# Optimization experiments

Measured on AMD Instinct MI355X. Metric: run time of the kernel, lower is better.

Reference implementation:

```python
import jax, jax.numpy as jnp
import numpy as np

NBINS = (128, 64, 32)
N_REGIONS = 5000
N_REGIONS_OI = 500
N_POINTS = 262144
SUM_H = sum(NBINS)            # 224
SUM_W = sum(n - 1 for n in NBINS)  # 221


def _spline_level(x, uw_region, uh_pt, local_ix):
    """One quadratic-spline level.
    x: [N] inputs in [0,1); uw_region: [R, n-1] region unnormalized widths;
    uh_pt: [N, n] per-point unnormalized heights (embedding + delta);
    local_ix: [N] int mapping points -> rows of uw_region.
    """
    # region-level widths / bin locations (calculate_widths / calculate_bin_locations)
    widths = jax.nn.softmax(uw_region, axis=-1)                # [R, n-1]
    bl = jnp.cumsum(widths, axis=-1)
    bl = bl.at[:, -1].set(1.0)
    bin_locations = jnp.pad(bl, ((0, 0), (1, 0)))              # [R, n]

    # gather per point (index_select(0, local_region_ix))
    widths_pt = widths[local_ix]                               # [N, n-1]
    bin_loc_pt = bin_locations[local_ix]                       # [N, n]

    # calculate_heights: exp then normalize so trapezoid integral == 1
    he = jnp.exp(uh_pt)                                        # [N, n]
    area = jnp.sum(0.5 * (he[:, :-1] + he[:, 1:]) * widths_pt, axis=-1, keepdims=True)
    heights = he / area                                        # [N, n]

    # calculate_bin_left_cdf
    cdf = jnp.cumsum(0.5 * (heights[:, :-1] + heights[:, 1:]) * widths_pt, axis=-1)
    cdf = cdf.at[:, -1].set(1.0)
    bin_left_cdf = jnp.pad(cdf, ((0, 0), (1, 0)))              # [N, n]

    # searchsorted(bin_locations, x, side='left') - 1, clamped to valid bins
    n = bin_loc_pt.shape[-1]
    bin_idx = jnp.clip(jnp.sum(bin_loc_pt < x[:, None], axis=-1) - 1, 0, n - 2)  # [N]

    take = lambda a, i: jnp.take_along_axis(a, i[:, None], axis=-1)[:, 0]
    in_loc = take(bin_loc_pt, bin_idx)
    in_w = take(widths_pt, bin_idx)
    in_cdf = take(bin_left_cdf, bin_idx)
    h_l = take(heights, bin_idx)
    h_r = take(heights, bin_idx + 1)

    alpha = (x - in_loc) / in_w
    a = 0.5 * (h_r - h_l) * in_w
    b = h_l * in_w
    out = a * alpha * alpha + b * alpha + in_cdf
    logabsdet = jnp.log(alpha * (h_r - h_l) + h_l)
    return out, logabsdet


def setup_inputs() -> dict:
    key = jax.random.key(0)
    k1, k2, k3, k4, k5, k6 = jax.random.split(key, 6)
    x = jax.random.uniform(k1, (N_POINTS,), dtype=jnp.float32)
    regions_oi = jax.random.randint(k2, (N_REGIONS_OI,), 0, N_REGIONS, dtype=jnp.int32)
    local_region_ix = jax.random.randint(k3, (N_POINTS,), 0, N_REGIONS_OI, dtype=jnp.int32)
    delta = jax.random.normal(k4, (N_POINTS, SUM_H), dtype=jnp.float32)
    # learned sparse embedding tables (init to random for a nontrivial baseline)
    heights_emb = 0.1 * jax.random.normal(k5, (N_REGIONS, SUM_H), dtype=jnp.float32)
    widths_emb = 0.1 * jax.random.normal(k6, (N_REGIONS, SUM_W), dtype=jnp.float32)
    return {"x": x, "regions_oi": regions_oi, "local_region_ix": local_region_ix,
            "delta": delta, "heights_emb": heights_emb, "widths_emb": widths_emb}


def reference(x, regions_oi, local_region_ix, delta, heights_emb, widths_emb):
    uh_all = heights_emb[regions_oi]   # [R, 224]
    uw_all = widths_emb[regions_oi]    # [R, 221]
    out = x
    logdet = jnp.zeros_like(x)
    oh = 0
    ow = 0
    for n in NBINS:
        uw = uw_all[:, ow:ow + (n - 1)]                               # [R, n-1]
        uh_pt = uh_all[local_region_ix][:, oh:oh + n] + delta[:, oh:oh + n]  # [N, n]
        out, ld = _spline_level(out, uw, uh_pt, local_region_ix)
        logdet = logdet + ld
        oh += n
        ow += n - 1
    return out, logdet
```

## Files before the change

kernel.cpp:

```cpp
#include <hip/hip_runtime.h>

#define NPOINTS 262144
#define SUMH 224
#define SUMW 221
#define NREG 500

__device__ __forceinline__ float rlane(float v, int l) {
  return __int_as_float(__builtin_amdgcn_readlane(__float_as_int(v), l));
}
template<int CTRL>
__device__ __forceinline__ float dpp0(float x) {
  return __int_as_float(__builtin_amdgcn_update_dpp(0, __float_as_int(x), CTRL, 0xF, 0xF, true));
}
template<int CTRL, int RM>
__device__ __forceinline__ float dpp_rm(float x) {
  return __int_as_float(__builtin_amdgcn_update_dpp(0, __float_as_int(x), CTRL, RM, 0xF, false));
}
template<int CTRL>
__device__ __forceinline__ float dpp_max_(float x) {
  return fmaxf(x, __int_as_float(__builtin_amdgcn_update_dpp(__float_as_int(x), __float_as_int(x), CTRL, 0xF, 0xF, false)));
}
__device__ __forceinline__ float wave_sum(float x) {
  x += dpp0<0x111>(x); x += dpp0<0x112>(x); x += dpp0<0x114>(x); x += dpp0<0x118>(x);
  x += dpp_rm<0x142, 0xA>(x); x += dpp_rm<0x143, 0xC>(x);
  return rlane(x, 63);
}
__device__ __forceinline__ float wave_max(float x) {
  x = dpp_max_<0x111>(x); x = dpp_max_<0x112>(x); x = dpp_max_<0x114>(x);
  x = dpp_max_<0x118>(x); x = dpp_max_<0x142>(x); x = dpp_max_<0x143>(x);
  return rlane(x, 63);
}
__device__ __forceinline__ float wave_scan_incl(float x) {
  x += dpp0<0x111>(x); x += dpp0<0x112>(x); x += dpp0<0x114>(x); x += dpp0<0x118>(x);
  x += dpp_rm<0x142, 0xA>(x);
  x += dpp_rm<0x143, 0xC>(x);
  return x;
}
__device__ __forceinline__ float grp32_sum(float x) {
  x += dpp0<0xB1>(x);
  x += dpp0<0x4E>(x);
  x += dpp0<0x141>(x);
  x += dpp0<0x140>(x);
  x += __int_as_float(__builtin_amdgcn_ds_swizzle(__float_as_int(x), 0x401F));
  return x;
}
__device__ __forceinline__ float bperm(int byteidx, float v) {
  return __int_as_float(__builtin_amdgcn_ds_bpermute(byteidx, __float_as_int(v)));
}


template<int M, int SRC, int DST, int NB>
__device__ __forceinline__ void region_level(const float* __restrict__ wrow,
    float* __restrict__ BL, float* __restrict__ HW, float* __restrict__ HS,
    int lane, float* lds)
{
  float v0 = (lane < M) ? wrow[SRC + lane] : -1e30f;
  float v1 = -1e30f;
  if constexpr (NB == 128) { if (lane + 64 < M) v1 = wrow[SRC + lane + 64]; }
  float m = wave_max(fmaxf(v0, v1));
  float e0 = __expf(v0 - m);
  float e1 = (NB == 128) ? __expf(v1 - m) : 0.0f;
  float s = wave_sum(e0 + e1);
  float inv = 1.0f / s;
  if (lane < NB) lds[lane] = e0;
  if constexpr (NB == 128) lds[lane + 64] = e1;
  __syncthreads();
  if (lane < NB) {
    HW[DST + lane] = 0.5f * e0 * inv;
    float prev = (lane == 0) ? 0.0f : lds[lane - 1];
    HS[DST + lane] = 0.5f * (e0 + prev) * inv;
  }
  if constexpr (NB == 128) {
    HW[DST + lane + 64] = 0.5f * e1 * inv;
    HS[DST + lane + 64] = 0.5f * (e1 + lds[lane + 63]) * inv;
  }
  float incl0 = wave_scan_incl(e0);
  if (lane == 0) BL[DST] = 0.0f;
  if (lane < M) BL[DST + 1 + lane] = (lane == M - 1) ? 1.0f : incl0 * inv;
  if constexpr (NB == 128) {
    float incl1 = wave_scan_incl(e1) + rlane(incl0, 63);
    int k = 64 + lane;
    if (k < M) BL[DST + 1 + k] = (k == M - 1) ? 1.0f : incl1 * inv;
  }
  __syncthreads();
}

__global__ void __launch_bounds__(64) region_kernel(
    const int* __restrict__ roi, const float* __restrict__ wemb,
    float* __restrict__ wsBL, float* __restrict__ wsHW, float* __restrict__ wsHS)
{
  __shared__ float lds[128];
  int rix = blockIdx.x;
  int lane = threadIdx.x;
  int greg = roi[rix];
  const float* wrow = wemb + (size_t)greg * SUMW;
  float* BL = wsBL + (size_t)rix * SUMH;
  float* HW = wsHW + (size_t)rix * SUMH;
  float* HS = wsHS + (size_t)rix * SUMH;
  region_level<127,   0,   0, 128>(wrow, BL, HW, HS, lane, lds);
  region_level< 63, 127, 128,  64>(wrow, BL, HW, HS, lane, lds);
  region_level< 31, 190, 192,  32>(wrow, BL, HW, HS, lane, lds);
}


template<int OFF, int C>
__device__ __forceinline__ void prep(const float* __restrict__ U,
    const float* __restrict__ D, const float* __restrict__ BLt,
    const float* __restrict__ HWt, const float* __restrict__ HSt, int s,
    float (&he)[C], float (&t)[C], float (&bl)[C], float (&hw)[C],
    float& larea, float& invarea)
{
  if constexpr (C == 4) {
    int c0 = OFF + s * 4;
    float4 a = *(const float4*)(U   + c0);
    float4 b = *(const float4*)(D   + c0);
    float4 e = *(const float4*)(BLt + c0);
    float4 f = *(const float4*)(HWt + c0);
    float4 g = *(const float4*)(HSt + c0);
    he[0] = __expf(a.x + b.x); he[1] = __expf(a.y + b.y);
    he[2] = __expf(a.z + b.z); he[3] = __expf(a.w + b.w);
    t[0] = he[0] * g.x; t[1] = he[1] * g.y; t[2] = he[2] * g.z; t[3] = he[3] * g.w;
    bl[0] = e.x; bl[1] = e.y; bl[2] = e.z; bl[3] = e.w;
    hw[0] = f.x; hw[1] = f.y; hw[2] = f.z; hw[3] = f.w;
  } else if constexpr (C == 2) {
    int c0 = OFF + s * 2;
    float2 a = *(const float2*)(U   + c0);
    float2 b = *(const float2*)(D   + c0);
    float2 e = *(const float2*)(BLt + c0);
    float2 f = *(const float2*)(HWt + c0);
    float2 g = *(const float2*)(HSt + c0);
    he[0] = __expf(a.x + b.x); he[1] = __expf(a.y + b.y);
    t[0] = he[0] * g.x; t[1] = he[1] * g.y;
    bl[0] = e.x; bl[1] = e.y; hw[0] = f.x; hw[1] = f.y;
  } else {
    int c0 = OFF + s;
    he[0] = __expf(U[c0] + D[c0]);
    t[0]  = he[0] * HSt[c0];
    bl[0] = BLt[c0];
    hw[0] = HWt[c0];
  }
  float a_ = 0.0f;
#pragma unroll
  for (int i = 0; i < C; ++i) a_ += t[i];
  float area = grp32_sum(a_);
  larea = __log2f(area);
  invarea = __builtin_amdgcn_rcpf(area);
}

template<int C>
__device__ __forceinline__ void apply(float& xv, float& logdet, int s, int nb_idx,
    const float (&he)[C], const float (&t)[C], const float (&bl)[C],
    const float (&hw)[C], float larea, float invarea)
{
  float f[C];
#pragma unroll
  for (int i = 0; i < C; ++i) f[i] = (bl[i] < xv) ? 1.0f : 0.0f;
  if (s == 0)  f[0]     = 1.0f;
  if (s == 31) f[C - 1] = 0.0f;
  float fN  = bperm(nb_idx, f[0]);
  float heN = bperm(nb_idx, he[0]);
  float hl = 0.0f, hr = 0.0f, loc = 0.0f, hwm = 0.0f, pt = 0.0f;
#pragma unroll
  for (int i = 0; i < C; ++i) {
    float fnext  = (i < C - 1) ? f[i + 1]  : fN;
    float henext = (i < C - 1) ? he[i + 1] : heN;
    float mi = f[i] * (1.0f - fnext);
    hl  += he[i] * mi;
    hr  += henext * mi;
    loc += bl[i] * mi;
    hwm += hw[i] * mi;
    pt  += t[i] * f[i];
  }
  hl  = grp32_sum(hl);
  hr  = grp32_sum(hr);
  loc = grp32_sum(loc);
  hwm = grp32_sum(hwm);
  pt  = grp32_sum(pt);
  float part = pt - hl * hwm;
  float inw = 2.0f * hwm;
  float alpha = (xv - loc) * __builtin_amdgcn_rcpf(inw);
  float dh = hr - hl;
  xv = ((0.5f * dh * alpha + hl) * alpha * inw + part) * invarea;
  logdet += (__log2f(alpha * dh + hl) - larea) * 0.69314718055994531f;
}

__global__ void __launch_bounds__(256, 8) spline_kernel(
    const float* __restrict__ x, const int* __restrict__ roi,
    const int* __restrict__ lix, const float* __restrict__ delta,
    const float* __restrict__ hemb,
    const float* __restrict__ wsBL, const float* __restrict__ wsHW,
    const float* __restrict__ wsHS, float* __restrict__ out)
{
  int tid  = (int)(blockIdx.x * blockDim.x + threadIdx.x);
  int wid  = tid >> 6;
  int lane = (int)(threadIdx.x & 63);
  int grp  = lane >> 5;
  int s    = lane & 31;
  int pid  = wid * 2 + grp;
  int nb_idx = ((lane + 1) & 63) << 2;

  float xv = x[pid];
  int r    = lix[pid];
  int greg = roi[r];
  const float* U   = hemb  + (size_t)greg * SUMH;
  const float* D   = delta + (size_t)pid  * SUMH;
  const float* BLt = wsBL  + (size_t)r    * SUMH;
  const float* HWt = wsHW  + (size_t)r    * SUMH;
  const float* HSt = wsHS  + (size_t)r    * SUMH;

  float he0[4], t0[4], bl0[4], hw0[4], la0, ia0;
  float he1[2], t1[2], bl1[2], hw1[2], la1, ia1;
  float he2[1], t2[1], bl2[1], hw2[1], la2, ia2;
  prep<  0, 4>(U, D, BLt, HWt, HSt, s, he0, t0, bl0, hw0, la0, ia0);
  prep<128, 2>(U, D, BLt, HWt, HSt, s, he1, t1, bl1, hw1, la1, ia1);
  prep<192, 1>(U, D, BLt, HWt, HSt, s, he2, t2, bl2, hw2, la2, ia2);

  float logdet = 0.0f;
  apply<4>(xv, logdet, s, nb_idx, he0, t0, bl0, hw0, la0, ia0);
  apply<2>(xv, logdet, s, nb_idx, he1, t1, bl1, hw1, la1, ia1);
  apply<1>(xv, logdet, s, nb_idx, he2, t2, bl2, hw2, la2, ia2);

  if (s == 0) {
    out[pid] = xv;
    out[NPOINTS + pid] = logdet;
  }
}


extern "C" void kernel_launch(void* const* d_in, const int* in_sizes, int n_in,
                              void* d_out, int out_size, void* d_ws, size_t ws_size,
                              hipStream_t stream) {
  const float* x     = (const float*)d_in[0];
  const int*   roi   = (const int*)  d_in[1];
  const int*   lix   = (const int*)  d_in[2];
  const float* delta = (const float*)d_in[3];
  const float* hemb  = (const float*)d_in[4];
  const float* wemb  = (const float*)d_in[5];

  float* wsBL = (float*)d_ws;
  float* wsHW = wsBL + (size_t)NREG * SUMH;
  float* wsHS = wsHW + (size_t)NREG * SUMH;

  region_kernel<<<NREG, 64, 0, stream>>>(roi, wemb, wsBL, wsHW, wsHS);
  spline_kernel<<<NPOINTS / 8, 256, 0, stream>>>(x, roi, lix, delta, hemb,
                                                 wsBL, wsHW, wsHS, (float*)d_out);
}
```

Measured before the change: 361.3 us.

## Process two points per half-wave with all loads issued before compute

Each wave now handles four points instead of two. All raw global loads for two points are issued up front into a register state struct, and then the spline math runs on each in turn, so more memory requests are in flight per wave. The exp/area computation moves from a separate prep step into the apply step. Launch bounds drop from 8 to 4 waves per SIMD and the grid is halved, trading occupancy for more loads per thread and higher register use.

```diff
diff --git a/kernel.cpp b/kernel.cpp
--- a/kernel.cpp
+++ b/kernel.cpp
@@ -48,7 +48,6 @@
   return __int_as_float(__builtin_amdgcn_ds_bpermute(byteidx, __float_as_int(v)));
 }
 
-
 template<int M, int SRC, int DST, int NB>
 __device__ __forceinline__ void region_level(const float* __restrict__ wrow,
     float* __restrict__ BL, float* __restrict__ HW, float* __restrict__ HS,
@@ -60,8 +59,8 @@
   float m = wave_max(fmaxf(v0, v1));
   float e0 = __expf(v0 - m);
   float e1 = (NB == 128) ? __expf(v1 - m) : 0.0f;
-  float s = wave_sum(e0 + e1);
-  float inv = 1.0f / s;
+  float sm = wave_sum(e0 + e1);
+  float inv = 1.0f / sm;
   if (lane < NB) lds[lane] = e0;
   if constexpr (NB == 128) lds[lane + 64] = e1;
   __syncthreads();
@@ -103,79 +102,76 @@
 }
 
 
-template<int OFF, int C>
-__device__ __forceinline__ void prep(const float* __restrict__ U,
-    const float* __restrict__ D, const float* __restrict__ BLt,
-    const float* __restrict__ HWt, const float* __restrict__ HSt, int s,
-    float (&he)[C], float (&t)[C], float (&bl)[C], float (&hw)[C],
-    float& larea, float& invarea)
-{
-  if constexpr (C == 4) {
-    int c0 = OFF + s * 4;
-    float4 a = *(const float4*)(U   + c0);
-    float4 b = *(const float4*)(D   + c0);
-    float4 e = *(const float4*)(BLt + c0);
-    float4 f = *(const float4*)(HWt + c0);
-    float4 g = *(const float4*)(HSt + c0);
-    he[0] = __expf(a.x + b.x); he[1] = __expf(a.y + b.y);
-    he[2] = __expf(a.z + b.z); he[3] = __expf(a.w + b.w);
-    t[0] = he[0] * g.x; t[1] = he[1] * g.y; t[2] = he[2] * g.z; t[3] = he[3] * g.w;
-    bl[0] = e.x; bl[1] = e.y; bl[2] = e.z; bl[3] = e.w;
-    hw[0] = f.x; hw[1] = f.y; hw[2] = f.z; hw[3] = f.w;
-  } else if constexpr (C == 2) {
-    int c0 = OFF + s * 2;
-    float2 a = *(const float2*)(U   + c0);
-    float2 b = *(const float2*)(D   + c0);
-    float2 e = *(const float2*)(BLt + c0);
-    float2 f = *(const float2*)(HWt + c0);
-    float2 g = *(const float2*)(HSt + c0);
-    he[0] = __expf(a.x + b.x); he[1] = __expf(a.y + b.y);
-    t[0] = he[0] * g.x; t[1] = he[1] * g.y;
-    bl[0] = e.x; bl[1] = e.y; hw[0] = f.x; hw[1] = f.y;
-  } else {
-    int c0 = OFF + s;
-    he[0] = __expf(U[c0] + D[c0]);
-    t[0]  = he[0] * HSt[c0];
-    bl[0] = BLt[c0];
-    hw[0] = HWt[c0];
-  }
-  float a_ = 0.0f;
+struct PtState {
+  float4 a0, b0, e0, f0, g0;
+  float2 a1, b1, e1, f1, g1;
+  float  a2, b2, e2, f2, g2;
+  float  xv;
+  int    pid;
+};
+
+__device__ __forceinline__ void load_pt(PtState& P, int pid, int s,
+    const float* __restrict__ x, const int* __restrict__ lix,
+    const int* __restrict__ roi, const float* __restrict__ delta,
+    const float* __restrict__ hemb, const float* __restrict__ wsBL,
+    const float* __restrict__ wsHW, const float* __restrict__ wsHS)
+{
+  P.pid = pid;
+  P.xv = x[pid];
+  int r = lix[pid];
+  int greg = roi[r];
+  const float* U  = hemb + (size_t)greg * SUMH;
+  const float* D  = delta + (size_t)pid * SUMH;
+  const float* BL = wsBL + (size_t)r * SUMH;
+  const float* HW = wsHW + (size_t)r * SUMH;
+  const float* HS = wsHS + (size_t)r * SUMH;
+  int c0 = s * 4;
+  P.a0 = *(const float4*)(U + c0);  P.b0 = *(const float4*)(D + c0);
+  P.e0 = *(const float4*)(BL + c0); P.f0 = *(const float4*)(HW + c0);
+  P.g0 = *(const float4*)(HS + c0);
+  int c1 = 128 + s * 2;
+  P.a1 = *(const float2*)(U + c1);  P.b1 = *(const float2*)(D + c1);
+  P.e1 = *(const float2*)(BL + c1); P.f1 = *(const float2*)(HW + c1);
+  P.g1 = *(const float2*)(HS + c1);
+  int c2 = 192 + s;
+  P.a2 = U[c2]; P.b2 = D[c2]; P.e2 = BL[c2]; P.f2 = HW[c2]; P.g2 = HS[c2];
+}
+
+template<int C>
+__device__ __forceinline__ void apply32(float& xv, float& logdet, int s, int nb_idx,
+    const float (&u)[C], const float (&d)[C], const float (&bl)[C],
+    const float (&hw)[C], const float (&hs)[C])
+{
+  float he[C], t[C], f[C];
 #pragma unroll
-  for (int i = 0; i < C; ++i) a_ += t[i];
-  float area = grp32_sum(a_);
-  larea = __log2f(area);
-  invarea = __builtin_amdgcn_rcpf(area);
-}
-
-template<int C>
-__device__ __forceinline__ void apply(float& xv, float& logdet, int s, int nb_idx,
-    const float (&he)[C], const float (&t)[C], const float (&bl)[C],
-    const float (&hw)[C], float larea, float invarea)
-{
-  float f[C];
+  for (int i = 0; i < C; ++i) { he[i] = __expf(u[i] + d[i]); t[i] = he[i] * hs[i]; }
 #pragma unroll
   for (int i = 0; i < C; ++i) f[i] = (bl[i] < xv) ? 1.0f : 0.0f;
   if (s == 0)  f[0]     = 1.0f;
   if (s == 31) f[C - 1] = 0.0f;
   float fN  = bperm(nb_idx, f[0]);
   float heN = bperm(nb_idx, he[0]);
-  float hl = 0.0f, hr = 0.0f, loc = 0.0f, hwm = 0.0f, pt = 0.0f;
+  float area = 0.0f, hl = 0.0f, hr = 0.0f, loc = 0.0f, hwm = 0.0f, pt = 0.0f;
 #pragma unroll
   for (int i = 0; i < C; ++i) {
     float fnext  = (i < C - 1) ? f[i + 1]  : fN;
     float henext = (i < C - 1) ? he[i + 1] : heN;
     float mi = f[i] * (1.0f - fnext);
+    area += t[i];
     hl  += he[i] * mi;
     hr  += henext * mi;
     loc += bl[i] * mi;
     hwm += hw[i] * mi;
     pt  += t[i] * f[i];
   }
+  area = grp32_sum(area);
   hl  = grp32_sum(hl);
   hr  = grp32_sum(hr);
   loc = grp32_sum(loc);
   hwm = grp32_sum(hwm);
   pt  = grp32_sum(pt);
+  float larea = __log2f(area);
+  float invarea = __builtin_amdgcn_rcpf(area);
   float part = pt - hl * hwm;
   float inw = 2.0f * hwm;
   float alpha = (xv - loc) * __builtin_amdgcn_rcpf(inw);
@@ -184,7 +180,42 @@
   logdet += (__log2f(alpha * dh + hl) - larea) * 0.69314718055994531f;
 }
 
-__global__ void __launch_bounds__(256, 8) spline_kernel(
+__device__ __forceinline__ void compute_pt(const PtState& P, int s, int nb_idx,
+                                           float* __restrict__ out)
+{
+  float xv = P.xv;
+  float logdet = 0.0f;
+  {
+    float u[4]  = {P.a0.x, P.a0.y, P.a0.z, P.a0.w};
+    float d[4]  = {P.b0.x, P.b0.y, P.b0.z, P.b0.w};
+    float bl[4] = {P.e0.x, P.e0.y, P.e0.z, P.e0.w};
+    float hw[4] = {P.f0.x, P.f0.y, P.f0.z, P.f0.w};
+    float hs[4] = {P.g0.x, P.g0.y, P.g0.z, P.g0.w};
+    apply32<4>(xv, logdet, s, nb_idx, u, d, bl, hw, hs);
+  }
+  {
+    float u[2]  = {P.a1.x, P.a1.y};
+    float d[2]  = {P.b1.x, P.b1.y};
+    float bl[2] = {P.e1.x, P.e1.y};
+    float hw[2] = {P.f1.x, P.f1.y};
+    float hs[2] = {P.g1.x, P.g1.y};
+    apply32<2>(xv, logdet, s, nb_idx, u, d, bl, hw, hs);
+  }
+  {
+    float u[1]  = {P.a2};
+    float d[1]  = {P.b2};
+    float bl[1] = {P.e2};
+    float hw[1] = {P.f2};
+    float hs[1] = {P.g2};
+    apply32<1>(xv, logdet, s, nb_idx, u, d, bl, hw, hs);
+  }
+  if (s == 0) {
+    out[P.pid] = xv;
+    out[NPOINTS + P.pid] = logdet;
+  }
+}
+
+__global__ void __launch_bounds__(256, 4) spline_kernel(
     const float* __restrict__ x, const int* __restrict__ roi,
     const int* __restrict__ lix, const float* __restrict__ delta,
     const float* __restrict__ hemb,
@@ -196,34 +227,15 @@
   int lane = (int)(threadIdx.x & 63);
   int grp  = lane >> 5;
   int s    = lane & 31;
-  int pid  = wid * 2 + grp;
+  int base = wid * 4;
   int nb_idx = ((lane + 1) & 63) << 2;
 
-  float xv = x[pid];
-  int r    = lix[pid];
-  int greg = roi[r];
-  const float* U   = hemb  + (size_t)greg * SUMH;
-  const float* D   = delta + (size_t)pid  * SUMH;
-  const float* BLt = wsBL  + (size_t)r    * SUMH;
-  const float* HWt = wsHW  + (size_t)r    * SUMH;
-  const float* HSt = wsHS  + (size_t)r    * SUMH;
-
-  float he0[4], t0[4], bl0[4], hw0[4], la0, ia0;
-  float he1[2], t1[2], bl1[2], hw1[2], la1, ia1;
-  float he2[1], t2[1], bl2[1], hw2[1], la2, ia2;
-  prep<  0, 4>(U, D, BLt, HWt, HSt, s, he0, t0, bl0, hw0, la0, ia0);
-  prep<128, 2>(U, D, BLt, HWt, HSt, s, he1, t1, bl1, hw1, la1, ia1);
-  prep<192, 1>(U, D, BLt, HWt, HSt, s, he2, t2, bl2, hw2, la2, ia2);
-
-  float logdet = 0.0f;
-  apply<4>(xv, logdet, s, nb_idx, he0, t0, bl0, hw0, la0, ia0);
-  apply<2>(xv, logdet, s, nb_idx, he1, t1, bl1, hw1, la1, ia1);
-  apply<1>(xv, logdet, s, nb_idx, he2, t2, bl2, hw2, la2, ia2);
-
-  if (s == 0) {
-    out[pid] = xv;
-    out[NPOINTS + pid] = logdet;
-  }
+  PtState A, B;
+  load_pt(A, base + grp,     s, x, lix, roi, delta, hemb, wsBL, wsHW, wsHS);
+  load_pt(B, base + 2 + grp, s, x, lix, roi, delta, hemb, wsBL, wsHW, wsHS);
+
+  compute_pt(A, s, nb_idx, out);
+  compute_pt(B, s, nb_idx, out);
 }
 
 
@@ -242,6 +254,6 @@
   float* wsHS = wsHW + (size_t)NREG * SUMH;
 
   region_kernel<<<NREG, 64, 0, stream>>>(roi, wemb, wsBL, wsHW, wsHS);
-  spline_kernel<<<NPOINTS / 8, 256, 0, stream>>>(x, roi, lix, delta, hemb,
-                                                 wsBL, wsHW, wsHS, (float*)d_out);
-}
+  spline_kernel<<<NPOINTS / 16, 256, 0, stream>>>(x, roi, lix, delta, hemb,
+                                                  wsBL, wsHW, wsHS, (float*)d_out);
+}
```

Result: faster. 347.0 us (-3.9%).
